# Kernel tuning notes

Hardware: AMD Instinct MI355X
Metric: run time of the kernel (lower is better)

## Reference

```python
import jax, jax.numpy as jnp
import numpy as np

NH, NKV, HD = 32, 8, 128   # query heads, kv heads, head_dim
EPS = 1e-6
ROPE_BASE = 10000.0


def setup_inputs() -> dict:
    key = jax.random.key(0)
    ks = jax.random.split(key, 5)
    B, S, H = 2, 1024, 4096
    scale = 0.02
    return {
        "x": jax.random.normal(ks[0], (B, S, H), jnp.float32),
        "wq": jax.random.normal(ks[1], (H, NH * HD), jnp.float32) * scale,
        "wk": jax.random.normal(ks[2], (H, NKV * HD), jnp.float32) * scale,
        "wv": jax.random.normal(ks[3], (H, NKV * HD), jnp.float32) * scale,
        "wo": jax.random.normal(ks[4], (NH * HD, H), jnp.float32) * scale,
        "q_norm_w": jnp.ones((HD,), jnp.float32),
        "k_norm_w": jnp.ones((HD,), jnp.float32),
    }


def _rmsnorm(t, w):
    # per-head RMSNorm over last dim (head_dim)
    var = jnp.mean(t * t, axis=-1, keepdims=True)
    return t * jax.lax.rsqrt(var + EPS) * w


def _rope(t, cos, sin):
    # t: [B,S,h,d]; cos/sin: [S, d/2] (neox / rotate-half style)
    d2 = t.shape[-1] // 2
    t1, t2 = t[..., :d2], t[..., d2:]
    c = cos[None, :, None, :]
    s = sin[None, :, None, :]
    return jnp.concatenate([t1 * c - t2 * s, t1 * s + t2 * c], axis=-1)


def reference(x, wq, wk, wv, wo, q_norm_w, k_norm_w):
    B, S, H = x.shape
    softmax_scale = HD ** (-0.5)

    q = (x @ wq).reshape(B, S, NH, HD)
    k = (x @ wk).reshape(B, S, NKV, HD)
    v = (x @ wv).reshape(B, S, NKV, HD)

    # QK RMSNorm (qwen3 use_qk_norm)
    q = _rmsnorm(q, q_norm_w)
    k = _rmsnorm(k, k_norm_w)

    # rotary embedding, base 10000
    inv_freq = 1.0 / (ROPE_BASE ** (jnp.arange(0, HD, 2, dtype=jnp.float32) / HD))
    ang = jnp.arange(S, dtype=jnp.float32)[:, None] * inv_freq[None, :]  # [S, d/2]
    cos, sin = jnp.cos(ang), jnp.sin(ang)
    q = _rope(q, cos, sin)
    k = _rope(k, cos, sin)

    # GQA: expand kv heads to match query heads
    g = NH // NKV
    k = jnp.repeat(k, g, axis=2)  # [B,S,NH,HD]
    v = jnp.repeat(v, g, axis=2)

    scores = jnp.einsum("bqhd,bkhd->bhqk", q, k) * softmax_scale
    causal = jnp.tril(jnp.ones((S, S), dtype=bool))
    scores = jnp.where(causal[None, None], scores, jnp.finfo(scores.dtype).min)
    probs = jax.nn.softmax(scores, axis=-1)
    ctx = jnp.einsum("bhqk,bkhd->bqhd", probs, v).reshape(B, S, NH * HD)
    return ctx @ wo
```

## Files before the change

### kernel.cpp

```cpp
#include <hip/hip_runtime.h>


#define NH_ 32
#define NKV_ 8
#define HD_ 128
#define SEQ_ 1024
#define HID_ 4096
#define NQKV_ 6144

typedef unsigned short u16;
typedef __bf16 bf16x8 __attribute__((ext_vector_type(8)));
typedef float f32x4 __attribute__((ext_vector_type(4)));

__device__ __forceinline__ u16 f2bf(float f) {
  unsigned int u = __float_as_uint(f);
  return (u16)((u + 0x7FFFu + ((u >> 16) & 1u)) >> 16);
}
__device__ __forceinline__ float bf2f(u16 u) {
  return __uint_as_float(((unsigned int)u) << 16);
}
__device__ __forceinline__ f32x4 mfma16(bf16x8 a, bf16x8 b, f32x4 c) {
  return __builtin_amdgcn_mfma_f32_16x16x32_bf16(a, b, c, 0, 0, 0);
}
__device__ __forceinline__ void gld16(u16* lds, const u16* g) {
  __builtin_amdgcn_global_load_lds(
      (const __attribute__((address_space(1))) unsigned int*)g,
      (__attribute__((address_space(3))) unsigned int*)lds, 16, 0, 0);
}

__global__ __launch_bounds__(256) void prep_all(
    const float* __restrict__ x, const float* __restrict__ wq,
    const float* __restrict__ wk, const float* __restrict__ wv,
    u16* __restrict__ xb, u16* __restrict__ wqkvt) {
  const int blk = blockIdx.x;
  if (blk < 4096) {
    int i = (blk * 256 + threadIdx.x) * 8;
    float4 a = *(const float4*)(x + i);
    float4 b = *(const float4*)(x + i + 4);
    u16 o[8];
    o[0] = f2bf(a.x); o[1] = f2bf(a.y); o[2] = f2bf(a.z); o[3] = f2bf(a.w);
    o[4] = f2bf(b.x); o[5] = f2bf(b.y); o[6] = f2bf(b.z); o[7] = f2bf(b.w);
    *(uint4*)(xb + i) = *(uint4*)&o[0];
    return;
  }
  __shared__ float t[32][33];
  const int tt = blk - 4096;
  const int k0 = (tt & 127) * 32;
  const int y = tt >> 7;
  const float* src;
  int ldn, n0;
  size_t dofs;
  if (y < 128) { src = wq; ldn = 4096; n0 = y * 32; dofs = 0; }
  else if (y < 160) { src = wk; ldn = 1024; n0 = (y - 128) * 32; dofs = (size_t)4096 * 4096; }
  else { src = wv; ldn = 1024; n0 = (y - 160) * 32; dofs = (size_t)5120 * 4096; }
  const int c = threadIdx.x & 31, r4 = threadIdx.x >> 5;
#pragma unroll
  for (int i = 0; i < 4; ++i) {
    int r = r4 + i * 8;
    t[r][c] = src[(size_t)(k0 + r) * ldn + n0 + c];
  }
  __syncthreads();
#pragma unroll
  for (int i = 0; i < 4; ++i) {
    int r = r4 + i * 8;
    wqkvt[dofs + (size_t)(n0 + r) * HID_ + k0 + c] = f2bf(t[c][r]);
  }
}

__global__ __launch_bounds__(256) void mid_all(
    const float* __restrict__ wo, const u16* __restrict__ QKV,
    const float* __restrict__ QW, const float* __restrict__ KW,
    u16* __restrict__ wot, u16* __restrict__ QB, u16* __restrict__ KB,
    u16* __restrict__ VT) {
  const int blk = blockIdx.x;
  if (blk < 16384) {
    __shared__ float t[32][33];
    const int k0 = (blk & 127) * 32, n0 = (blk >> 7) * 32;
    const int c = threadIdx.x & 31, r4 = threadIdx.x >> 5;
#pragma unroll
    for (int i = 0; i < 4; ++i) {
      int r = r4 + i * 8;
      t[r][c] = wo[(size_t)(k0 + r) * HID_ + n0 + c];
    }
    __syncthreads();
#pragma unroll
    for (int i = 0; i < 4; ++i) {
      int r = r4 + i * 8;
      wot[(size_t)(n0 + r) * HID_ + k0 + c] = f2bf(t[c][r]);
    }
    return;
  }
  if (blk < 36864) {
    const float QSCALE = 0.08838834764831845f * 1.4426950408889634f;
    int vec = (blk - 16384) * 4 + (threadIdx.x >> 6);
    int lane = threadIdx.x & 63;
    const u16* src;
    u16* dst;
    const float* nw;
    int m;
    float outsc;
    if (vec < 65536) {
      m = vec >> 5;
      int hh = vec & 31;
      src = QKV + (size_t)m * NQKV_ + hh * 128;
      int b = m >> 10, s = m & 1023;
      dst = QB + (size_t)((b * NH_ + hh) * SEQ_ + s) * HD_;
      nw = QW;
      outsc = QSCALE;
    } else {
      int vk = vec - 65536;
      m = vk >> 3;
      int kvh = vk & 7;
      src = QKV + (size_t)m * NQKV_ + 4096 + kvh * 128;
      int b = m >> 10, s = m & 1023;
      dst = KB + (size_t)((b * NKV_ + kvh) * SEQ_ + s) * HD_;
      nw = KW;
      outsc = 1.0f;
    }
    float t1 = bf2f(src[lane]), t2 = bf2f(src[lane + 64]);
    float ss = t1 * t1 + t2 * t2;
#pragma unroll
    for (int off = 32; off >= 1; off >>= 1) ss += __shfl_xor(ss, off);
    float scale = rsqrtf(ss * (1.0f / 128.0f) + 1e-6f) * outsc;
    float n1 = t1 * scale * nw[lane];
    float n2 = t2 * scale * nw[lane + 64];
    int spos = m & 1023;
    float invf = powf(10000.0f, -(float)lane * (1.0f / 64.0f));
    float ang = (float)spos * invf;
    float sn, cs;
    sincosf(ang, &sn, &cs);
    dst[lane] = f2bf(n1 * cs - n2 * sn);
    dst[lane + 64] = f2bf(n1 * sn + n2 * cs);
    return;
  }
  {
    __shared__ u16 t[32][33];
    const int tt = blk - 36864;
    const int s0 = (tt & 31) * 32, d0 = ((tt >> 5) & 3) * 32;
    const int bkvh = tt >> 7;
    const int b = bkvh >> 3, kvh = bkvh & 7;
    const int c = threadIdx.x & 31, r8 = threadIdx.x >> 5;
#pragma unroll
    for (int i = 0; i < 4; ++i) {
      int r = r8 + i * 8;
      t[r][c] =
          QKV[(size_t)(b * SEQ_ + s0 + r) * NQKV_ + 5120 + kvh * 128 + d0 + c];
    }
    __syncthreads();
#pragma unroll
    for (int i = 0; i < 4; ++i) {
      int r = r8 + i * 8;
      VT[(size_t)(bkvh * HD_ + d0 + r) * SEQ_ + s0 + c] = t[c][r];
    }
  }
}


#define BAR() __builtin_amdgcn_s_barrier()
#define PRIO1() __builtin_amdgcn_s_setprio(1)
#define PRIO0() __builtin_amdgcn_s_setprio(0)
#define VM(n) asm volatile("s_waitcnt vmcnt(" #n ")" ::: "memory")

#define STGA(slot, l, koff) \
  gld16(&L[(slot)*SLOT + (l)*4096 + wofs], aB + (size_t)(l)*64*K + (koff))
#define STGB(slot, l, koff) \
  gld16(&L[(slot)*SLOT + 8192 + (l)*4096 + wofs], bB + (size_t)(l)*64*K + (koff))

#define RDB(dst, Ls, p)                                                   \
  dst[0][0] = *(const bf16x8*)&(Ls)[bro + (2*(p))*4096 + acS0];           \
  dst[0][1] = *(const bf16x8*)&(Ls)[bro + (2*(p)+1)*4096 + acS0];         \
  dst[1][0] = *(const bf16x8*)&(Ls)[bro + (2*(p))*4096 + acS1];           \
  dst[1][1] = *(const bf16x8*)&(Ls)[bro + (2*(p)+1)*4096 + acS1];

#define RDA(dst, Ls)                                                      \
  _Pragma("unroll") for (int m_ = 0; m_ < 4; ++m_) {                      \
    dst[0][m_] = *(const bf16x8*)&(Ls)[aro + m_*1024 + acS0];             \
    dst[1][m_] = *(const bf16x8*)&(Ls)[aro + m_*1024 + acS1];             \
  }

#define MMp(p, bq, AF)                                                    \
  _Pragma("unroll") for (int kk = 0; kk < 2; ++kk)                        \
  _Pragma("unroll") for (int m = 0; m < 4; ++m)                           \
  _Pragma("unroll") for (int j = 0; j < 2; ++j)                           \
    acc[m][2*(p)+j] = mfma16(AF[kk][m], bq[kk][j], acc[m][2*(p)+j]);

#define TILE3(SO, SN, AFc, AFn, K1, K2)                                   \
  {                                                                       \
    const u16* Ls = &L[(SO)*SLOT];                                        \
    bf16x8 bq0[2][2], bq1[2][2], bq2[2][2];                               \
    RDB(bq0, Ls, 0); RDB(bq1, Ls, 1);                                     \
    STGB((SN), 4, (K1)); STGB((SN), 5, (K1));                             \
    BAR(); PRIO1(); MMp(0, bq0, AFc); PRIO0(); BAR();                     \
    RDB(bq2, Ls, 2);                                                      \
    STGA((SO), 0, (K2)); STGA((SO), 1, (K2)); STGB((SO), 0, (K2));        \
    BAR(); PRIO1(); MMp(1, bq1, AFc); PRIO0(); VM(8); BAR();              \
    RDA(AFn, (&L[(SN)*SLOT]));                                            \
    STGB((SO), 1, (K2)); STGB((SO), 2, (K2)); STGB((SO), 3, (K2));        \
    BAR(); PRIO1(); MMp(2, bq2, AFc); PRIO0(); VM(6); BAR();              \
  }

#define TILE2(SO, SN, AFc, AFn, K1, K2)                                   \
  {                                                                       \
    const u16* Ls = &L[(SO)*SLOT];                                        \
    bf16x8 bq0[2][2], bq1[2][2];                                          \
    RDB(bq0, Ls, 0); RDB(bq1, Ls, 1);                                     \
    STGB((SN), 2, (K1)); STGB((SN), 3, (K1));                             \
    BAR(); PRIO1(); MMp(0, bq0, AFc); PRIO0(); VM(2); BAR();              \
    RDA(AFn, (&L[(SN)*SLOT]));                                            \
    STGA((SO), 0, (K2)); STGA((SO), 1, (K2));                             \
    STGB((SO), 0, (K2)); STGB((SO), 1, (K2));                             \
    BAR(); PRIO1(); MMp(1, bq1, AFc); PRIO0(); VM(4); BAR();              \
  }

template <int NF, bool F32OUT>
__global__ __launch_bounds__(512, 2) void gemm8p(
    const u16* __restrict__ A_, const u16* __restrict__ Bt,
    void* __restrict__ Cv, const int K, const int ldc) {
  constexpr int NP = NF / 2;
  constexpr int SLOT = (128 + NF * 64) * 64;
  __shared__ __align__(16) u16 L[2 * SLOT];

  const int sw = (blockIdx.x & 7) * 32 + (blockIdx.x >> 3);
  const int bm = sw >> 4, bn = sw & 15;

  const int tid = threadIdx.x, w = tid >> 6, lane = tid & 63;
  const int wm = w >> 2, wn = w & 3;
  const int ln = lane & 15, quad = lane >> 4;

  const int srow = lane >> 3;
  const int scol = ((lane & 7) ^ srow) * 8;
  const u16* aB = A_ + (size_t)(bm * 128 + w * 8 + srow) * K + scol;
  const u16* bB = Bt + (size_t)(bn * (NF * 64) + w * 8 + srow) * K + scol;
  const int wofs = w * 512;

  const int acS0 = (quad * 8) ^ ((ln & 7) << 3);
  const int acS1 = (32 + quad * 8) ^ ((ln & 7) << 3);
  const int aro = (wm * 64 + ln) * 64;
  const int bro = 8192 + (wn * 16 + ln) * 64;

  f32x4 acc[4][NF];
#pragma unroll
  for (int m = 0; m < 4; ++m)
#pragma unroll
    for (int f = 0; f < NF; ++f)
#pragma unroll
      for (int r = 0; r < 4; ++r) acc[m][f][r] = 0.0f;

  const int nt = K >> 6;
  bf16x8 af0[2][4], af1[2][4];

  if constexpr (NP == 3) {
    STGA(0, 0, 0); STGA(0, 1, 0);
    STGB(0, 0, 0); STGB(0, 1, 0); STGB(0, 2, 0);
    STGB(0, 3, 0); STGB(0, 4, 0); STGB(0, 5, 0);
    STGA(1, 0, 64); STGA(1, 1, 64); STGB(1, 0, 64);
    STGB(1, 1, 64); STGB(1, 2, 64); STGB(1, 3, 64);
    VM(6); BAR();
    RDA(af0, (&L[0]));
    int kof = 0;
#pragma unroll 1
    for (int it = 0; it < (nt - 2) / 2; ++it) {
      TILE3(0, 1, af0, af1, kof + 64, kof + 128);
      TILE3(1, 0, af1, af0, kof + 128, kof + 192);
      kof += 128;
    }
    {
      const u16* Ls = &L[0];
      bf16x8 bq0[2][2], bq1[2][2], bq2[2][2];
      RDB(bq0, Ls, 0); RDB(bq1, Ls, 1);
      STGB(1, 4, kof + 64); STGB(1, 5, kof + 64);
      BAR(); PRIO1(); MMp(0, bq0, af0); PRIO0(); BAR();
      RDB(bq2, Ls, 2);
      BAR(); PRIO1(); MMp(1, bq1, af0); PRIO0(); VM(5); BAR();
      RDA(af1, (&L[SLOT]));
      BAR(); PRIO1(); MMp(2, bq2, af0); PRIO0(); VM(0); BAR();
    }
    {
      const u16* Ls = &L[SLOT];
      bf16x8 bq0[2][2], bq1[2][2], bq2[2][2];
      RDB(bq0, Ls, 0); RDB(bq1, Ls, 1); RDB(bq2, Ls, 2);
      BAR();
      PRIO1();
      MMp(0, bq0, af1); MMp(1, bq1, af1); MMp(2, bq2, af1);
      PRIO0();
    }
  } else {
    STGA(0, 0, 0); STGA(0, 1, 0);
    STGB(0, 0, 0); STGB(0, 1, 0); STGB(0, 2, 0); STGB(0, 3, 0);
    STGA(1, 0, 64); STGA(1, 1, 64); STGB(1, 0, 64); STGB(1, 1, 64);
    VM(4); BAR();
    RDA(af0, (&L[0]));
    int kof = 0;
#pragma unroll 1
    for (int it = 0; it < (nt - 2) / 2; ++it) {
      TILE2(0, 1, af0, af1, kof + 64, kof + 128);
      TILE2(1, 0, af1, af0, kof + 128, kof + 192);
      kof += 128;
    }
    {
      const u16* Ls = &L[0];
      bf16x8 bq0[2][2], bq1[2][2];
      RDB(bq0, Ls, 0); RDB(bq1, Ls, 1);
      STGB(1, 2, kof + 64); STGB(1, 3, kof + 64);
      BAR(); PRIO1(); MMp(0, bq0, af0); PRIO0(); VM(2); BAR();
      RDA(af1, (&L[SLOT]));
      BAR(); PRIO1(); MMp(1, bq1, af0); PRIO0(); VM(0); BAR();
    }
    {
      const u16* Ls = &L[SLOT];
      bf16x8 bq0[2][2], bq1[2][2];
      RDB(bq0, Ls, 0); RDB(bq1, Ls, 1);
      BAR();
      PRIO1();
      MMp(0, bq0, af1); MMp(1, bq1, af1);
      PRIO0();
    }
  }

  const int colb = bn * (NF * 64) + wn * 16 + ln;
#pragma unroll
  for (int m = 0; m < 4; ++m) {
#pragma unroll
    for (int r = 0; r < 4; ++r) {
      const int grow = bm * 128 + wm * 64 + m * 16 + quad * 4 + r;
      if (F32OUT) {
        float* dst = (float*)Cv + (size_t)grow * ldc + colb;
#pragma unroll
        for (int f = 0; f < NF; ++f) dst[f * 64] = acc[m][f][r];
      } else {
        u16* dst = (u16*)Cv + (size_t)grow * ldc + colb;
#pragma unroll
        for (int f = 0; f < NF; ++f) dst[f * 64] = f2bf(acc[m][f][r]);
      }
    }
  }
}

#undef TILE3
#undef TILE2
#undef RDB
#undef RDA
#undef MMp
#undef STGA
#undef STGB
#undef BAR
#undef PRIO1
#undef PRIO0
#undef VM

__global__ __launch_bounds__(256) void flash_attn(
    const u16* __restrict__ QB, const u16* __restrict__ KB,
    const u16* __restrict__ VT, u16* __restrict__ CTX) {
  __shared__ u16 Ks[4][64][32];
  __shared__ u16 Vs[2][128][32];
  __shared__ u16 Pl[4][16][72];

  const int bid = blockIdx.x;
  const int qt = 15 - (bid >> 6);
  const int h = bid & 31, b = (bid >> 5) & 1;
  const int kvh = h >> 2;
  const int tid = threadIdx.x, w = tid >> 6, lane = tid & 63;
  const int ln = lane & 15, quad = lane >> 4;
  const int l4 = lane >> 2, l4r = lane & 3;

  const u16* qbase =
      QB + (size_t)((b * NH_ + h) * SEQ_ + qt * 64 + w * 16 + ln) * HD_;
  bf16x8 qf[4];
#pragma unroll
  for (int kc = 0; kc < 4; ++kc)
    qf[kc] = *(const bf16x8*)(qbase + kc * 32 + quad * 8);

  f32x4 o[8];
#pragma unroll
  for (int t = 0; t < 8; ++t)
#pragma unroll
    for (int r = 0; r < 4; ++r) o[t][r] = 0.0f;
  float m_r[4] = {-3e38f, -3e38f, -3e38f, -3e38f};
  float l_r[4] = {0.0f, 0.0f, 0.0f, 0.0f};

  const u16* krow =
      KB + (size_t)((b * NKV_ + kvh) * SEQ_ + w * 16 + l4) * HD_ + l4r * 8;
  const u16* vrow =
      VT + (size_t)((b * NKV_ + kvh) * HD_ + w * 32 + l4) * SEQ_ + l4r * 8;
  const int pswz = ((ln >> 3) & 1) << 3;

  for (int kt = 0; kt <= qt; ++kt) {
    const int key0 = kt * 64;
#pragma unroll
    for (int i = 0; i < 4; ++i)
      gld16(&Ks[i][w * 16][0], krow + (size_t)key0 * HD_ + i * 32);
#pragma unroll
    for (int i = 0; i < 4; ++i)
      gld16(&Vs[i & 1][w * 32 + (i >> 1) * 16][0],
            vrow + (size_t)(i >> 1) * 16 * SEQ_ + key0 + (i & 1) * 32);
    __syncthreads();

    f32x4 sc[4];
#pragma unroll
    for (int t2 = 0; t2 < 4; ++t2) {
#pragma unroll
      for (int r = 0; r < 4; ++r) sc[t2][r] = 0.0f;
#pragma unroll
      for (int kc = 0; kc < 4; ++kc) {
        bf16x8 kf = *(const bf16x8*)&Ks[kc][t2 * 16 + ln][quad * 8];
        sc[t2] = mfma16(qf[kc], kf, sc[t2]);
      }
    }

    const bool diag = (kt == qt);
    float p[4][4], alpha[4];
#pragma unroll
    for (int r = 0; r < 4; ++r) {
      float s0 = sc[0][r], s1 = sc[1][r], s2 = sc[2][r], s3 = sc[3][r];
      if (diag) {
        const int qi = qt * 64 + w * 16 + quad * 4 + r;
        if (key0 + ln > qi) s0 = -3e38f;
        if (key0 + 16 + ln > qi) s1 = -3e38f;
        if (key0 + 32 + ln > qi) s2 = -3e38f;
        if (key0 + 48 + ln > qi) s3 = -3e38f;
      }
      float mx = fmaxf(fmaxf(s0, s1), fmaxf(s2, s3));
#pragma unroll
      for (int off = 1; off < 16; off <<= 1) mx = fmaxf(mx, __shfl_xor(mx, off));
      float mnew = fmaxf(m_r[r], mx);
      alpha[r] = exp2f(m_r[r] - mnew);
      p[0][r] = exp2f(s0 - mnew);
      p[1][r] = exp2f(s1 - mnew);
      p[2][r] = exp2f(s2 - mnew);
      p[3][r] = exp2f(s3 - mnew);
      float rs = p[0][r] + p[1][r] + p[2][r] + p[3][r];
#pragma unroll
      for (int off = 1; off < 16; off <<= 1) rs += __shfl_xor(rs, off);
      l_r[r] = l_r[r] * alpha[r] + rs;
      m_r[r] = mnew;
    }
#pragma unroll
    for (int t = 0; t < 8; ++t)
#pragma unroll
      for (int r = 0; r < 4; ++r) o[t][r] *= alpha[r];

#pragma unroll
    for (int r = 0; r < 4; ++r) {
      const int row = quad * 4 + r;
      const int wswz = ((row >> 3) & 1) << 3;
#pragma unroll
      for (int t2 = 0; t2 < 4; ++t2)
        Pl[w][row][(t2 * 16 + ln) ^ wswz] = f2bf(p[t2][r]);
    }
    bf16x8 af0 = *(const bf16x8*)&Pl[w][ln][(quad * 8) ^ pswz];
    bf16x8 af1 = *(const bf16x8*)&Pl[w][ln][32 + ((quad * 8) ^ pswz)];
#pragma unroll
    for (int t = 0; t < 8; ++t) {
      bf16x8 vf0 = *(const bf16x8*)&Vs[0][t * 16 + ln][quad * 8];
      o[t] = mfma16(af0, vf0, o[t]);
      bf16x8 vf1 = *(const bf16x8*)&Vs[1][t * 16 + ln][quad * 8];
      o[t] = mfma16(af1, vf1, o[t]);
    }
    __syncthreads();
  }

#pragma unroll
  for (int r = 0; r < 4; ++r) {
    float inv_l = 1.0f / l_r[r];
    int srow = qt * 64 + w * 16 + quad * 4 + r;
    u16* dst = CTX + (size_t)(b * SEQ_ + srow) * (NH_ * HD_) + h * HD_;
#pragma unroll
    for (int t = 0; t < 8; ++t) dst[t * 16 + ln] = f2bf(o[t][r] * inv_l);
  }
}

extern "C" void kernel_launch(void* const* d_in, const int* in_sizes, int n_in,
                              void* d_out, int out_size, void* d_ws,
                              size_t ws_size, hipStream_t stream) {
  const float* x = (const float*)d_in[0];
  const float* wq = (const float*)d_in[1];
  const float* wk = (const float*)d_in[2];
  const float* wv = (const float*)d_in[3];
  const float* wo = (const float*)d_in[4];
  const float* qw = (const float*)d_in[5];
  const float* kw = (const float*)d_in[6];
  float* out = (float*)d_out;
  char* ws = (char*)d_ws;
  const size_t MB = 1024 * 1024;

  u16* wqkvt = (u16*)ws;
  u16* wot = (u16*)ws;
  u16* xb = (u16*)(ws + 48 * MB);
  u16* qkv = (u16*)(ws + 64 * MB);
  u16* ctx = (u16*)(ws + 64 * MB);
  u16* qb = (u16*)(ws + 88 * MB);
  u16* kb = (u16*)(ws + 104 * MB);
  u16* vt = (u16*)(ws + 108 * MB);

  prep_all<<<dim3(28672), 256, 0, stream>>>(x, wq, wk, wv, xb, wqkvt);
  gemm8p<6, false><<<dim3(256), 512, 0, stream>>>(xb, wqkvt, qkv, 4096, 6144);
  mid_all<<<dim3(38912), 256, 0, stream>>>(wo, qkv, qw, kw, wot, qb, kb, vt);
  flash_attn<<<dim3(1024), 256, 0, stream>>>(qb, kb, vt, ctx);
  gemm8p<4, true><<<dim3(256), 512, 0, stream>>>(ctx, wot, out, 4096, 4096);
}
```

Measured before the change: 448.7 us.

## Switch GEMMs to 4-wave blocks with half-width N tiles and doubled grid

Both projection GEMMs move from 8-wave blocks with 128xNF*64 tiles to 4-wave blocks with 128xNF*32 tiles. The grid doubles to 512 blocks, and the global-to-LDS staging, LDS fragment reads and vmcnt waits are reshuffled to fit the smaller tile. With 256 CUs, 512 blocks should spread work more evenly and use a smaller LDS footprint per block. The cost is lower reuse of each A tile per block, and the hand-tuned wait counts carry a correctness risk.

```diff
diff --git a/kernel.cpp b/kernel.cpp
--- a/kernel.cpp
+++ b/kernel.cpp
@@ -161,16 +161,18 @@
 #define PRIO0() __builtin_amdgcn_s_setprio(0)
 #define VM(n) asm volatile("s_waitcnt vmcnt(" #n ")" ::: "memory")
 
-#define STGA(slot, l, koff) \
-  gld16(&L[(slot)*SLOT + (l)*4096 + wofs], aB + (size_t)(l)*64*K + (koff))
-#define STGB(slot, l, koff) \
-  gld16(&L[(slot)*SLOT + 8192 + (l)*4096 + wofs], bB + (size_t)(l)*64*K + (koff))
+#define STGA(slot, l, h, koff)                                            \
+  gld16(&L[(slot)*SLOT + (l)*4096 + (w + (h)*4)*512],                     \
+        aB + (size_t)((l)*64 + (w + (h)*4)*8)*K + (koff))
+#define STGB(slot, l, h, koff)                                            \
+  gld16(&L[(slot)*SLOT + 8192 + (l)*4096 + (w + (h)*4)*512],              \
+        bB + (size_t)((l)*64 + (w + (h)*4)*8)*K + (koff))
 
 #define RDB(dst, Ls, p)                                                   \
-  dst[0][0] = *(const bf16x8*)&(Ls)[bro + (2*(p))*4096 + acS0];           \
-  dst[0][1] = *(const bf16x8*)&(Ls)[bro + (2*(p)+1)*4096 + acS0];         \
-  dst[1][0] = *(const bf16x8*)&(Ls)[bro + (2*(p))*4096 + acS1];           \
-  dst[1][1] = *(const bf16x8*)&(Ls)[bro + (2*(p)+1)*4096 + acS1];
+  dst[0][0] = *(const bf16x8*)&(Ls)[bro + (p)*4096 + acS0];               \
+  dst[0][1] = *(const bf16x8*)&(Ls)[bro + (p)*4096 + 2048 + acS0];        \
+  dst[1][0] = *(const bf16x8*)&(Ls)[bro + (p)*4096 + acS1];               \
+  dst[1][1] = *(const bf16x8*)&(Ls)[bro + (p)*4096 + 2048 + acS1];
 
 #define RDA(dst, Ls)                                                      \
   _Pragma("unroll") for (int m_ = 0; m_ < 4; ++m_) {                      \
@@ -189,13 +191,15 @@
     const u16* Ls = &L[(SO)*SLOT];                                        \
     bf16x8 bq0[2][2], bq1[2][2], bq2[2][2];                               \
     RDB(bq0, Ls, 0); RDB(bq1, Ls, 1);                                     \
-    STGB((SN), 4, (K1)); STGB((SN), 5, (K1));                             \
-    BAR(); PRIO1(); MMp(0, bq0, AFc); PRIO0(); BAR();                     \
+    STGB((SN), 0, 0, (K1)); STGB((SN), 0, 1, (K1));                       \
+    BAR(); PRIO1(); MMp(0, bq0, AFc); PRIO0(); VM(6); BAR();              \
     RDB(bq2, Ls, 2);                                                      \
-    STGA((SO), 0, (K2)); STGA((SO), 1, (K2)); STGB((SO), 0, (K2));        \
-    BAR(); PRIO1(); MMp(1, bq1, AFc); PRIO0(); VM(8); BAR();              \
+    STGB((SN), 1, 0, (K1)); STGB((SN), 1, 1, (K1));                       \
+    STGB((SN), 2, 0, (K1)); STGB((SN), 2, 1, (K1));                       \
+    BAR(); PRIO1(); MMp(1, bq1, AFc); PRIO0(); VM(6); BAR();              \
     RDA(AFn, (&L[(SN)*SLOT]));                                            \
-    STGB((SO), 1, (K2)); STGB((SO), 2, (K2)); STGB((SO), 3, (K2));        \
+    STGA((SO), 0, 0, (K2)); STGA((SO), 0, 1, (K2));                       \
+    STGA((SO), 1, 0, (K2)); STGA((SO), 1, 1, (K2));                       \
     BAR(); PRIO1(); MMp(2, bq2, AFc); PRIO0(); VM(6); BAR();              \
   }
 
@@ -204,34 +208,35 @@
     const u16* Ls = &L[(SO)*SLOT];                                        \
     bf16x8 bq0[2][2], bq1[2][2];                                          \
     RDB(bq0, Ls, 0); RDB(bq1, Ls, 1);                                     \
-    STGB((SN), 2, (K1)); STGB((SN), 3, (K1));                             \
-    BAR(); PRIO1(); MMp(0, bq0, AFc); PRIO0(); VM(2); BAR();              \
+    STGB((SN), 0, 0, (K1)); STGB((SN), 0, 1, (K1));                       \
+    STGB((SN), 1, 0, (K1)); STGB((SN), 1, 1, (K1));                       \
+    BAR(); PRIO1(); MMp(0, bq0, AFc); PRIO0(); VM(4); BAR();              \
     RDA(AFn, (&L[(SN)*SLOT]));                                            \
-    STGA((SO), 0, (K2)); STGA((SO), 1, (K2));                             \
-    STGB((SO), 0, (K2)); STGB((SO), 1, (K2));                             \
+    STGA((SO), 0, 0, (K2)); STGA((SO), 0, 1, (K2));                       \
+    STGA((SO), 1, 0, (K2)); STGA((SO), 1, 1, (K2));                       \
     BAR(); PRIO1(); MMp(1, bq1, AFc); PRIO0(); VM(4); BAR();              \
   }
 
 template <int NF, bool F32OUT>
-__global__ __launch_bounds__(512, 2) void gemm8p(
+__global__ __launch_bounds__(256, 2) void gemm4w(
     const u16* __restrict__ A_, const u16* __restrict__ Bt,
     void* __restrict__ Cv, const int K, const int ldc) {
   constexpr int NP = NF / 2;
-  constexpr int SLOT = (128 + NF * 64) * 64;
+  constexpr int BN = NF * 32;
+  constexpr int SLOT = (2 + NP) * 4096;
   __shared__ __align__(16) u16 L[2 * SLOT];
 
-  const int sw = (blockIdx.x & 7) * 32 + (blockIdx.x >> 3);
-  const int bm = sw >> 4, bn = sw & 15;
+  const int sw = (blockIdx.x & 7) * 64 + (blockIdx.x >> 3);
+  const int bm = sw >> 5, bn = sw & 31;
 
   const int tid = threadIdx.x, w = tid >> 6, lane = tid & 63;
-  const int wm = w >> 2, wn = w & 3;
+  const int wm = w >> 1, wn = w & 1;
   const int ln = lane & 15, quad = lane >> 4;
 
   const int srow = lane >> 3;
   const int scol = ((lane & 7) ^ srow) * 8;
-  const u16* aB = A_ + (size_t)(bm * 128 + w * 8 + srow) * K + scol;
-  const u16* bB = Bt + (size_t)(bn * (NF * 64) + w * 8 + srow) * K + scol;
-  const int wofs = w * 512;
+  const u16* aB = A_ + (size_t)(bm * 128 + srow) * K + scol;
+  const u16* bB = Bt + (size_t)(bn * BN + srow) * K + scol;
 
   const int acS0 = (quad * 8) ^ ((ln & 7) << 3);
   const int acS1 = (32 + quad * 8) ^ ((ln & 7) << 3);
@@ -250,11 +255,11 @@
   bf16x8 af0[2][4], af1[2][4];
 
   if constexpr (NP == 3) {
-    STGA(0, 0, 0); STGA(0, 1, 0);
-    STGB(0, 0, 0); STGB(0, 1, 0); STGB(0, 2, 0);
-    STGB(0, 3, 0); STGB(0, 4, 0); STGB(0, 5, 0);
-    STGA(1, 0, 64); STGA(1, 1, 64); STGB(1, 0, 64);
-    STGB(1, 1, 64); STGB(1, 2, 64); STGB(1, 3, 64);
+    STGA(0, 0, 0, 0); STGA(0, 0, 1, 0); STGA(0, 1, 0, 0); STGA(0, 1, 1, 0);
+    STGB(0, 0, 0, 0); STGB(0, 0, 1, 0);
+    STGB(0, 1, 0, 0); STGB(0, 1, 1, 0);
+    STGB(0, 2, 0, 0); STGB(0, 2, 1, 0);
+    STGA(1, 0, 0, 64); STGA(1, 0, 1, 64); STGA(1, 1, 0, 64); STGA(1, 1, 1, 64);
     VM(6); BAR();
     RDA(af0, (&L[0]));
     int kof = 0;
@@ -268,26 +273,29 @@
       const u16* Ls = &L[0];
       bf16x8 bq0[2][2], bq1[2][2], bq2[2][2];
       RDB(bq0, Ls, 0); RDB(bq1, Ls, 1);
-      STGB(1, 4, kof + 64); STGB(1, 5, kof + 64);
-      BAR(); PRIO1(); MMp(0, bq0, af0); PRIO0(); BAR();
+      STGB(1, 0, 0, kof + 64); STGB(1, 0, 1, kof + 64);
+      BAR(); PRIO1(); MMp(0, bq0, af0); PRIO0(); VM(6); BAR();
       RDB(bq2, Ls, 2);
-      BAR(); PRIO1(); MMp(1, bq1, af0); PRIO0(); VM(5); BAR();
+      STGB(1, 1, 0, kof + 64); STGB(1, 1, 1, kof + 64);
+      STGB(1, 2, 0, kof + 64); STGB(1, 2, 1, kof + 64);
+      BAR(); PRIO1(); MMp(1, bq1, af0); PRIO0(); VM(6); BAR();
       RDA(af1, (&L[SLOT]));
-      BAR(); PRIO1(); MMp(2, bq2, af0); PRIO0(); VM(0); BAR();
+      BAR(); PRIO1(); MMp(2, bq2, af0); PRIO0(); VM(2); BAR();
     }
     {
       const u16* Ls = &L[SLOT];
       bf16x8 bq0[2][2], bq1[2][2], bq2[2][2];
-      RDB(bq0, Ls, 0); RDB(bq1, Ls, 1); RDB(bq2, Ls, 2);
+      RDB(bq0, Ls, 0); RDB(bq1, Ls, 1);
+      BAR(); PRIO1(); MMp(0, bq0, af1); PRIO0(); VM(0); BAR();
+      RDB(bq2, Ls, 2);
       BAR();
-      PRIO1();
-      MMp(0, bq0, af1); MMp(1, bq1, af1); MMp(2, bq2, af1);
-      PRIO0();
+      PRIO1(); MMp(1, bq1, af1); MMp(2, bq2, af1); PRIO0();
     }
   } else {
-    STGA(0, 0, 0); STGA(0, 1, 0);
-    STGB(0, 0, 0); STGB(0, 1, 0); STGB(0, 2, 0); STGB(0, 3, 0);
-    STGA(1, 0, 64); STGA(1, 1, 64); STGB(1, 0, 64); STGB(1, 1, 64);
+    STGA(0, 0, 0, 0); STGA(0, 0, 1, 0); STGA(0, 1, 0, 0); STGA(0, 1, 1, 0);
+    STGB(0, 0, 0, 0); STGB(0, 0, 1, 0);
+    STGB(0, 1, 0, 0); STGB(0, 1, 1, 0);
+    STGA(1, 0, 0, 64); STGA(1, 0, 1, 64); STGA(1, 1, 0, 64); STGA(1, 1, 1, 64);
     VM(4); BAR();
     RDA(af0, (&L[0]));
     int kof = 0;
@@ -301,8 +309,9 @@
       const u16* Ls = &L[0];
       bf16x8 bq0[2][2], bq1[2][2];
       RDB(bq0, Ls, 0); RDB(bq1, Ls, 1);
-      STGB(1, 2, kof + 64); STGB(1, 3, kof + 64);
-      BAR(); PRIO1(); MMp(0, bq0, af0); PRIO0(); VM(2); BAR();
+      STGB(1, 0, 0, kof + 64); STGB(1, 0, 1, kof + 64);
+      STGB(1, 1, 0, kof + 64); STGB(1, 1, 1, kof + 64);
+      BAR(); PRIO1(); MMp(0, bq0, af0); PRIO0(); VM(4); BAR();
       RDA(af1, (&L[SLOT]));
       BAR(); PRIO1(); MMp(1, bq1, af0); PRIO0(); VM(0); BAR();
     }
@@ -311,13 +320,11 @@
       bf16x8 bq0[2][2], bq1[2][2];
       RDB(bq0, Ls, 0); RDB(bq1, Ls, 1);
       BAR();
-      PRIO1();
-      MMp(0, bq0, af1); MMp(1, bq1, af1);
-      PRIO0();
-    }
-  }
-
-  const int colb = bn * (NF * 64) + wn * 16 + ln;
+      PRIO1(); MMp(0, bq0, af1); MMp(1, bq1, af1); PRIO0();
+    }
+  }
+
+  const int colb = bn * BN + wn * 16 + ln;
 #pragma unroll
   for (int m = 0; m < 4; ++m) {
 #pragma unroll
@@ -326,11 +333,11 @@
       if (F32OUT) {
         float* dst = (float*)Cv + (size_t)grow * ldc + colb;
 #pragma unroll
-        for (int f = 0; f < NF; ++f) dst[f * 64] = acc[m][f][r];
+        for (int f = 0; f < NF; ++f) dst[f * 32] = acc[m][f][r];
       } else {
         u16* dst = (u16*)Cv + (size_t)grow * ldc + colb;
 #pragma unroll
-        for (int f = 0; f < NF; ++f) dst[f * 64] = f2bf(acc[m][f][r]);
+        for (int f = 0; f < NF; ++f) dst[f * 32] = f2bf(acc[m][f][r]);
       }
     }
   }
@@ -493,8 +500,8 @@
   u16* vt = (u16*)(ws + 108 * MB);
 
   prep_all<<<dim3(28672), 256, 0, stream>>>(x, wq, wk, wv, xb, wqkvt);
-  gemm8p<6, false><<<dim3(256), 512, 0, stream>>>(xb, wqkvt, qkv, 4096, 6144);
+  gemm4w<6, false><<<dim3(512), 256, 0, stream>>>(xb, wqkvt, qkv, 4096, 6144);
   mid_all<<<dim3(38912), 256, 0, stream>>>(wo, qkv, qw, kw, wot, qb, kb, vt);
   flash_attn<<<dim3(1024), 256, 0, stream>>>(qb, kb, vt, ctx);
-  gemm8p<4, true><<<dim3(256), 512, 0, stream>>>(ctx, wot, out, 4096, 4096);
-}
+  gemm4w<4, true><<<dim3(512), 256, 0, stream>>>(ctx, wot, out, 4096, 4096);
+}
```

Measured after the change: 495.5 us. 10.4% more time.

## Restructure GEMM pipeline: triple-buffer LDS for NF=4, simplify single-fragment schedule

Applied to the files above, without the earlier changes.

Replaces the unrolled two-tile ping-pong GEMM with a simpler per-tile loop that uses one A-fragment set and one B-fragment set, adding explicit lgkmcnt waits before each MFMA phase. The NF=4 output projection moves to three LDS slots with prefetch two tiles ahead. The NF=6 QKV projection keeps two slots but now issues loads one tile ahead inside the loop. The goal is lower register pressure and more global-load latency hiding. The cost is that A fragments are no longer prefetched across tiles, and the LDS footprint grows for NF=4, which could limit occupancy at 2 blocks per CU.

```diff
diff --git a/kernel.cpp b/kernel.cpp
--- a/kernel.cpp
+++ b/kernel.cpp
@@ -159,6 +159,7 @@
 #define BAR() __builtin_amdgcn_s_barrier()
 #define PRIO1() __builtin_amdgcn_s_setprio(1)
 #define PRIO0() __builtin_amdgcn_s_setprio(0)
+#define LGKM0() asm volatile("s_waitcnt lgkmcnt(0)" ::: "memory")
 #define VM(n) asm volatile("s_waitcnt vmcnt(" #n ")" ::: "memory")
 
 #define STGA(slot, l, koff) \
@@ -166,59 +167,31 @@
 #define STGB(slot, l, koff) \
   gld16(&L[(slot)*SLOT + 8192 + (l)*4096 + wofs], bB + (size_t)(l)*64*K + (koff))
 
-#define RDB(dst, Ls, p)                                                   \
-  dst[0][0] = *(const bf16x8*)&(Ls)[bro + (2*(p))*4096 + acS0];           \
-  dst[0][1] = *(const bf16x8*)&(Ls)[bro + (2*(p)+1)*4096 + acS0];         \
-  dst[1][0] = *(const bf16x8*)&(Ls)[bro + (2*(p))*4096 + acS1];           \
-  dst[1][1] = *(const bf16x8*)&(Ls)[bro + (2*(p)+1)*4096 + acS1];
-
-#define RDA(dst, Ls)                                                      \
+#define RDB(Ls, p)                                                        \
+  bq[0][0] = *(const bf16x8*)&(Ls)[bro + (2*(p))*4096 + acS0];            \
+  bq[0][1] = *(const bf16x8*)&(Ls)[bro + (2*(p)+1)*4096 + acS0];          \
+  bq[1][0] = *(const bf16x8*)&(Ls)[bro + (2*(p))*4096 + acS1];            \
+  bq[1][1] = *(const bf16x8*)&(Ls)[bro + (2*(p)+1)*4096 + acS1];
+
+#define RDA(Ls)                                                           \
   _Pragma("unroll") for (int m_ = 0; m_ < 4; ++m_) {                      \
-    dst[0][m_] = *(const bf16x8*)&(Ls)[aro + m_*1024 + acS0];             \
-    dst[1][m_] = *(const bf16x8*)&(Ls)[aro + m_*1024 + acS1];             \
-  }
-
-#define MMp(p, bq, AF)                                                    \
+    af[0][m_] = *(const bf16x8*)&(Ls)[aro + m_*1024 + acS0];              \
+    af[1][m_] = *(const bf16x8*)&(Ls)[aro + m_*1024 + acS1];              \
+  }
+
+#define MMp(p)                                                            \
   _Pragma("unroll") for (int kk = 0; kk < 2; ++kk)                        \
   _Pragma("unroll") for (int m = 0; m < 4; ++m)                           \
   _Pragma("unroll") for (int j = 0; j < 2; ++j)                           \
-    acc[m][2*(p)+j] = mfma16(AF[kk][m], bq[kk][j], acc[m][2*(p)+j]);
-
-#define TILE3(SO, SN, AFc, AFn, K1, K2)                                   \
-  {                                                                       \
-    const u16* Ls = &L[(SO)*SLOT];                                        \
-    bf16x8 bq0[2][2], bq1[2][2], bq2[2][2];                               \
-    RDB(bq0, Ls, 0); RDB(bq1, Ls, 1);                                     \
-    STGB((SN), 4, (K1)); STGB((SN), 5, (K1));                             \
-    BAR(); PRIO1(); MMp(0, bq0, AFc); PRIO0(); BAR();                     \
-    RDB(bq2, Ls, 2);                                                      \
-    STGA((SO), 0, (K2)); STGA((SO), 1, (K2)); STGB((SO), 0, (K2));        \
-    BAR(); PRIO1(); MMp(1, bq1, AFc); PRIO0(); VM(8); BAR();              \
-    RDA(AFn, (&L[(SN)*SLOT]));                                            \
-    STGB((SO), 1, (K2)); STGB((SO), 2, (K2)); STGB((SO), 3, (K2));        \
-    BAR(); PRIO1(); MMp(2, bq2, AFc); PRIO0(); VM(6); BAR();              \
-  }
-
-#define TILE2(SO, SN, AFc, AFn, K1, K2)                                   \
-  {                                                                       \
-    const u16* Ls = &L[(SO)*SLOT];                                        \
-    bf16x8 bq0[2][2], bq1[2][2];                                          \
-    RDB(bq0, Ls, 0); RDB(bq1, Ls, 1);                                     \
-    STGB((SN), 2, (K1)); STGB((SN), 3, (K1));                             \
-    BAR(); PRIO1(); MMp(0, bq0, AFc); PRIO0(); VM(2); BAR();              \
-    RDA(AFn, (&L[(SN)*SLOT]));                                            \
-    STGA((SO), 0, (K2)); STGA((SO), 1, (K2));                             \
-    STGB((SO), 0, (K2)); STGB((SO), 1, (K2));                             \
-    BAR(); PRIO1(); MMp(1, bq1, AFc); PRIO0(); VM(4); BAR();              \
-  }
+    acc[m][2*(p)+j] = mfma16(af[kk][m], bq[kk][j], acc[m][2*(p)+j]);
 
 template <int NF, bool F32OUT>
-__global__ __launch_bounds__(512, 2) void gemm8p(
+__global__ __launch_bounds__(512, 2) void gemm3p(
     const u16* __restrict__ A_, const u16* __restrict__ Bt,
     void* __restrict__ Cv, const int K, const int ldc) {
-  constexpr int NP = NF / 2;
-  constexpr int SLOT = (128 + NF * 64) * 64;
-  __shared__ __align__(16) u16 L[2 * SLOT];
+  constexpr int NSLOT = (NF == 4) ? 3 : 2;
+  constexpr int SLOT = (2 + NF) * 4096;
+  __shared__ __align__(16) u16 L[NSLOT * SLOT];
 
   const int sw = (blockIdx.x & 7) * 32 + (blockIdx.x >> 3);
   const int bm = sw >> 4, bn = sw & 15;
@@ -247,73 +220,71 @@
       for (int r = 0; r < 4; ++r) acc[m][f][r] = 0.0f;
 
   const int nt = K >> 6;
-  bf16x8 af0[2][4], af1[2][4];
-
-  if constexpr (NP == 3) {
+  bf16x8 af[2][4], bq[2][2];
+
+  if constexpr (NF == 6) {
     STGA(0, 0, 0); STGA(0, 1, 0);
     STGB(0, 0, 0); STGB(0, 1, 0); STGB(0, 2, 0);
     STGB(0, 3, 0); STGB(0, 4, 0); STGB(0, 5, 0);
-    STGA(1, 0, 64); STGA(1, 1, 64); STGB(1, 0, 64);
-    STGB(1, 1, 64); STGB(1, 2, 64); STGB(1, 3, 64);
-    VM(6); BAR();
-    RDA(af0, (&L[0]));
-    int kof = 0;
+    VM(4); BAR();
 #pragma unroll 1
-    for (int it = 0; it < (nt - 2) / 2; ++it) {
-      TILE3(0, 1, af0, af1, kof + 64, kof + 128);
-      TILE3(1, 0, af1, af0, kof + 128, kof + 192);
-      kof += 128;
+    for (int t = 0; t < nt - 1; ++t) {
+      const u16* Ls = &L[(t & 1) * SLOT];
+      const int sn = (t + 1) & 1;
+      const int k1 = (t + 1) << 6;
+      RDA(Ls); RDB(Ls, 0);
+      STGA(sn, 0, k1); STGA(sn, 1, k1); STGB(sn, 0, k1); STGB(sn, 1, k1);
+      BAR(); LGKM0(); PRIO1(); MMp(0); PRIO0(); VM(6); BAR();
+      RDB(Ls, 1);
+      STGB(sn, 2, k1); STGB(sn, 3, k1);
+      BAR(); LGKM0(); PRIO1(); MMp(1); PRIO0(); VM(6); BAR();
+      RDB(Ls, 2);
+      STGB(sn, 4, k1); STGB(sn, 5, k1);
+      BAR(); LGKM0(); PRIO1(); MMp(2); PRIO0(); VM(4); BAR();
     }
     {
-      const u16* Ls = &L[0];
-      bf16x8 bq0[2][2], bq1[2][2], bq2[2][2];
-      RDB(bq0, Ls, 0); RDB(bq1, Ls, 1);
-      STGB(1, 4, kof + 64); STGB(1, 5, kof + 64);
-      BAR(); PRIO1(); MMp(0, bq0, af0); PRIO0(); BAR();
-      RDB(bq2, Ls, 2);
-      BAR(); PRIO1(); MMp(1, bq1, af0); PRIO0(); VM(5); BAR();
-      RDA(af1, (&L[SLOT]));
-      BAR(); PRIO1(); MMp(2, bq2, af0); PRIO0(); VM(0); BAR();
-    }
-    {
-      const u16* Ls = &L[SLOT];
-      bf16x8 bq0[2][2], bq1[2][2], bq2[2][2];
-      RDB(bq0, Ls, 0); RDB(bq1, Ls, 1); RDB(bq2, Ls, 2);
-      BAR();
-      PRIO1();
-      MMp(0, bq0, af1); MMp(1, bq1, af1); MMp(2, bq2, af1);
-      PRIO0();
+      const u16* Ls = &L[((nt - 1) & 1) * SLOT];
+      RDA(Ls); RDB(Ls, 0);
+      BAR(); LGKM0(); PRIO1(); MMp(0); PRIO0(); VM(2); BAR();
+      RDB(Ls, 1);
+      BAR(); LGKM0(); PRIO1(); MMp(1); PRIO0(); VM(0); BAR();
+      RDB(Ls, 2);
+      BAR(); LGKM0(); PRIO1(); MMp(2); PRIO0();
     }
   } else {
     STGA(0, 0, 0); STGA(0, 1, 0);
     STGB(0, 0, 0); STGB(0, 1, 0); STGB(0, 2, 0); STGB(0, 3, 0);
-    STGA(1, 0, 64); STGA(1, 1, 64); STGB(1, 0, 64); STGB(1, 1, 64);
-    VM(4); BAR();
-    RDA(af0, (&L[0]));
-    int kof = 0;
+    STGA(1, 0, 64); STGA(1, 1, 64);
+    STGB(1, 0, 64); STGB(1, 1, 64); STGB(1, 2, 64); STGB(1, 3, 64);
+    VM(6); BAR();
+    int so = 0;
 #pragma unroll 1
-    for (int it = 0; it < (nt - 2) / 2; ++it) {
-      TILE2(0, 1, af0, af1, kof + 64, kof + 128);
-      TILE2(1, 0, af1, af0, kof + 128, kof + 192);
-      kof += 128;
+    for (int t = 0; t < nt - 2; ++t) {
+      const u16* Ls = &L[so * SLOT];
+      const int sn = (so == 0) ? 2 : so - 1;
+      const int k2 = (t + 2) << 6;
+      RDA(Ls); RDB(Ls, 0);
+      STGA(sn, 0, k2); STGA(sn, 1, k2); STGB(sn, 0, k2); STGB(sn, 1, k2);
+      BAR(); LGKM0(); PRIO1(); MMp(0); PRIO0(); BAR();
+      RDB(Ls, 1);
+      STGB(sn, 2, k2); STGB(sn, 3, k2);
+      BAR(); LGKM0(); PRIO1(); MMp(1); PRIO0(); VM(6); BAR();
+      so = (so == 2) ? 0 : so + 1;
     }
     {
-      const u16* Ls = &L[0];
-      bf16x8 bq0[2][2], bq1[2][2];
-      RDB(bq0, Ls, 0); RDB(bq1, Ls, 1);
-      STGB(1, 2, kof + 64); STGB(1, 3, kof + 64);
-      BAR(); PRIO1(); MMp(0, bq0, af0); PRIO0(); VM(2); BAR();
-      RDA(af1, (&L[SLOT]));
-      BAR(); PRIO1(); MMp(1, bq1, af0); PRIO0(); VM(0); BAR();
+      const u16* Ls = &L[so * SLOT];
+      RDA(Ls); RDB(Ls, 0);
+      BAR(); LGKM0(); PRIO1(); MMp(0); PRIO0(); BAR();
+      RDB(Ls, 1);
+      BAR(); LGKM0(); PRIO1(); MMp(1); PRIO0(); VM(0); BAR();
+      so = (so == 2) ? 0 : so + 1;
     }
     {
-      const u16* Ls = &L[SLOT];
-      bf16x8 bq0[2][2], bq1[2][2];
-      RDB(bq0, Ls, 0); RDB(bq1, Ls, 1);
-      BAR();
-      PRIO1();
-      MMp(0, bq0, af1); MMp(1, bq1, af1);
-      PRIO0();
+      const u16* Ls = &L[so * SLOT];
+      RDA(Ls); RDB(Ls, 0);
+      BAR(); LGKM0(); PRIO1(); MMp(0); PRIO0(); BAR();
+      RDB(Ls, 1);
+      BAR(); LGKM0(); PRIO1(); MMp(1); PRIO0();
     }
   }
 
@@ -336,8 +307,6 @@
   }
 }
 
-#undef TILE3
-#undef TILE2
 #undef RDB
 #undef RDA
 #undef MMp
@@ -346,6 +315,7 @@
 #undef BAR
 #undef PRIO1
 #undef PRIO0
+#undef LGKM0
 #undef VM
 
 __global__ __launch_bounds__(256) void flash_attn(
@@ -493,8 +463,8 @@
   u16* vt = (u16*)(ws + 108 * MB);
 
   prep_all<<<dim3(28672), 256, 0, stream>>>(x, wq, wk, wv, xb, wqkvt);
-  gemm8p<6, false><<<dim3(256), 512, 0, stream>>>(xb, wqkvt, qkv, 4096, 6144);
+  gemm3p<6, false><<<dim3(256), 512, 0, stream>>>(xb, wqkvt, qkv, 4096, 6144);
   mid_all<<<dim3(38912), 256, 0, stream>>>(wo, qkv, qw, kw, wot, qb, kb, vt);
   flash_attn<<<dim3(1024), 256, 0, stream>>>(qb, kb, vt, ctx);
-  gemm8p<4, true><<<dim3(256), 512, 0, stream>>>(ctx, wot, out, 4096, 4096);
-}
+  gemm3p<4, true><<<dim3(256), 512, 0, stream>>>(ctx, wot, out, 4096, 4096);
+}
```

Result: no change. 454.3 us (+1.2%).
